# Optimization experiments

Measured on AMD Instinct MI355X. Metric: run time of the kernel, lower is better.

The kernel has to match this reference:

```python
import jax, jax.numpy as jnp
import numpy as np

B, S, T = 32, 2048, 768
NH, DH, DHID = 8, 96, 384  # num_heads, head_dim, hidden_dim=4*head_dim


def setup_inputs() -> dict:
    key = jax.random.key(0)
    k = jax.random.split(key, 7)
    token_embeddings = jax.random.normal(k[0], (B, S, T), dtype=jnp.float32)
    attention_mask = jnp.ones((B, S), dtype=jnp.float32)
    # per-head Linear params, stacked on a leading head axis (PyTorch default-ish init scale)
    P_w = jax.random.normal(k[1], (NH, T, DH), dtype=jnp.float32) * (1.0 / np.sqrt(T))
    P_b = jax.random.normal(k[2], (NH, DH), dtype=jnp.float32) * 0.01
    W1_w = jax.random.normal(k[3], (NH, DH, DHID), dtype=jnp.float32) * (1.0 / np.sqrt(DH))
    W1_b = jax.random.normal(k[4], (NH, DHID), dtype=jnp.float32) * 0.01
    W2_w = jax.random.normal(k[5], (NH, DHID, DH), dtype=jnp.float32) * (1.0 / np.sqrt(DHID))
    W2_b = jax.random.normal(k[6], (NH, DH), dtype=jnp.float32) * 0.01
    return {
        'token_embeddings': token_embeddings,
        'attention_mask': attention_mask,
        'P_w': P_w, 'P_b': P_b,
        'W1_w': W1_w, 'W1_b': W1_b,
        'W2_w': W2_w, 'W2_b': W2_b,
    }


def reference(token_embeddings, attention_mask, P_w, P_b, W1_w, W1_b, W2_w, W2_b):
    # Batched over heads instead of the original Python loop; same math per head.
    # H_i = P_i(H): (B, NH, S, DH)
    Hi = jnp.einsum('bst,htd->bhsd', token_embeddings, P_w) + P_b[None, :, None, :]
    # A_i = W2_i(relu(W1_i(H_i))): (B, NH, S, DH)
    A = jax.nn.relu(jnp.einsum('bhsd,hde->bhse', Hi, W1_w) + W1_b[None, :, None, :])
    A = jnp.einsum('bhse,hed->bhsd', A, W2_w) + W2_b[None, :, None, :]
    # masked softmax over the sequence axis (log(mask) adds -inf at padded tokens)
    log_mask = jnp.log(attention_mask)[:, None, :, None]  # (B,1,S,1)
    A = jax.nn.softmax(A + log_mask, axis=2)
    # weighted sum over tokens: (B, NH, DH)
    v = jnp.sum(Hi * A, axis=2)
    # concat heads -> (B, NH*DH) == (B, sentence_dim)
    return v.reshape(v.shape[0], NH * DH)
```

## Files before the change

kernel.cpp:

```cpp
#include <hip/hip_runtime.h>
#include <cstdint>
#include <cstddef>

#define Bsz   32
#define Ssz   2048
#define Tsz   768
#define NH    8
#define DH    96
#define DHID  384
#define Ncols (NH*DH)

using u16 = unsigned short;
typedef __bf16 bf16x8 __attribute__((ext_vector_type(8)));
typedef __bf16 bf16x4 __attribute__((ext_vector_type(4)));
typedef float  f32x4  __attribute__((ext_vector_type(4)));

__device__ __forceinline__ u16 f2bn(float f) {
  __bf16 h = (__bf16)f;
  return __builtin_bit_cast(u16, h);
}
__device__ __forceinline__ float b2f(u16 u) {
  return __builtin_bit_cast(float, (uint32_t)u << 16);
}

typedef const __attribute__((address_space(1))) void* gas_t;
typedef __attribute__((address_space(3))) void* las_t;
__device__ __forceinline__ void gload16(const void* g, void* s) {
  __builtin_amdgcn_global_load_lds((gas_t)g, (las_t)s, 16, 0, 0);
}

__global__ __launch_bounds__(256) void k_pack(const float* __restrict__ Pw,
    const float* __restrict__ W1w, const float* __restrict__ W2w,
    u16* __restrict__ B1t, u16* __restrict__ W1t, u16* __restrict__ W2t)
{
  int i = blockIdx.x * 256 + threadIdx.x;
  if (i < 589824) {
    int n = i / 768, k = i % 768;
    int h = n / 96, d = n % 96;
    B1t[i] = f2bn(Pw[(size_t)h*73728 + (size_t)k*96 + d]);
  } else if (i < 589824 + 294912) {
    int j = i - 589824;
    int h = j / 36864, r = j % 36864;
    int n = r / 96, k = r % 96;
    W1t[j] = f2bn(W1w[(size_t)h*36864 + (size_t)k*384 + n]);
  } else if (i < 589824 + 2*294912) {
    int q = i - 589824 - 294912;
    int h = q / 36864, r = q % 36864;
    int n = r / 384, k = r % 384;
    W2t[q] = f2bn(W2w[(size_t)h*36864 + (size_t)k*96 + n]);
  }
}

__global__ __launch_bounds__(256, 2) void k_gemm1(const float* __restrict__ emb,
    const u16* __restrict__ B1t, const float* __restrict__ Pb, u16* __restrict__ Hi)
{
  __shared__ u16 As[256*64];
  __shared__ u16 Bs[128*64];
  const int tid  = threadIdx.x;
  const int lane = tid & 63;
  const int w    = tid >> 6;
  const int wr = w >> 1, wc = w & 1;
  const int L = blockIdx.x;
  const int widx = (L & 7) * 192 + (L >> 3);
  const int bm = widx / 6, bn = widx % 6;
  const int l15 = lane & 15, lg = lane >> 4;

  const int srow   = lane >> 3;
  const int schunk = lane & 7;
  const int brow_in = lane >> 3;
  const int bchunk  = lane & 7;

  f32x4 acc[8][4] = {};

  for (int kt = 0; kt < 12; ++kt) {
    const int k0 = kt * 64;
    #pragma unroll
    for (int i = 0; i < 4; ++i) {
      const int row = (w*4 + i)*8 + brow_in;
      const int lc  = bchunk ^ brow_in;
      gload16(B1t + (size_t)(bn*128 + row)*Tsz + k0 + lc*8,
              &Bs[(w*4 + i)*512]);
    }
    #pragma unroll
    for (int i = 0; i < 8; ++i) {
      const int row = w*64 + i*8 + srow;
      const float* src = emb + (size_t)(bm*256 + row)*Tsz + k0 + schunk*8;
      float4 v0 = *reinterpret_cast<const float4*>(src);
      float4 v1 = *reinterpret_cast<const float4*>(src + 4);
      bf16x8 af;
      af[0] = (__bf16)v0.x; af[1] = (__bf16)v0.y; af[2] = (__bf16)v0.z; af[3] = (__bf16)v0.w;
      af[4] = (__bf16)v1.x; af[5] = (__bf16)v1.y; af[6] = (__bf16)v1.z; af[7] = (__bf16)v1.w;
      const int phys = schunk ^ (row & 7);
      *reinterpret_cast<bf16x8*>(&As[row*64 + phys*8]) = af;
    }
    __syncthreads();

    #pragma unroll
    for (int kk = 0; kk < 2; ++kk) {
      const int clog = kk*4 + lg;
      bf16x8 b[4];
      #pragma unroll
      for (int c = 0; c < 4; ++c) {
        const int Rb = wc*64 + c*16 + l15;
        b[c] = *reinterpret_cast<const bf16x8*>(&Bs[Rb*64 + (clog ^ (Rb & 7))*8]);
      }
      bf16x8 a[8];
      #pragma unroll
      for (int m = 0; m < 8; ++m) {
        const int R = wr*128 + m*16 + l15;
        a[m] = *reinterpret_cast<const bf16x8*>(&As[R*64 + (clog ^ (R & 7))*8]);
      }
      #pragma unroll
      for (int m = 0; m < 8; ++m)
        #pragma unroll
        for (int c = 0; c < 4; ++c)
          acc[m][c] = __builtin_amdgcn_mfma_f32_16x16x32_bf16(a[m], b[c], acc[m][c], 0, 0, 0);
    }
    __syncthreads();
  }
  #pragma unroll
  for (int c = 0; c < 4; ++c) {
    int col = bn*128 + wc*64 + c*16 + l15;
    float bias = Pb[col];
    #pragma unroll
    for (int m = 0; m < 8; ++m) {
      int row0 = bm*256 + wr*128 + m*16 + lg*4;
      #pragma unroll
      for (int j = 0; j < 4; ++j)
        Hi[(size_t)(row0 + j)*Ncols + col] = f2bn(acc[m][c][j] + bias);
    }
  }
}

__global__ __launch_bounds__(256, 1) void k_ffn_pool(
    const u16* __restrict__ Hi, const u16* __restrict__ W1t, const u16* __restrict__ W2t,
    const float* __restrict__ b1, const float* __restrict__ b2v, const float* __restrict__ mask,
    float* __restrict__ out)
{
  __shared__ u16 W2s[96][392];
  __shared__ u16 Zb[4][2][16][40];
  __shared__ float mb[4][96], lb[4][96], ab[4][96];

  const int tid = threadIdx.x, lane = tid & 63, w = tid >> 6;
  const int l15 = lane & 15, lg = lane >> 4;
  const int h = blockIdx.x, b = blockIdx.y;

  const u16* W1h = W1t + (size_t)h * DHID * DH;
  const u16* W2h = W2t + (size_t)h * DH * DHID;
  const float* b1h = b1 + h * DHID;

  for (int i = tid; i < 96*48; i += 256) {
    int r = i / 48, g = i % 48;
    uint4 v = *reinterpret_cast<const uint4*>(W2h + (size_t)r*DHID + g*8);
    *reinterpret_cast<uint4*>(&W2s[r][g*8]) = v;
  }
  __syncthreads();

  float b2s[6];
  #pragma unroll
  for (int ct = 0; ct < 6; ++ct) b2s[ct] = b2v[h*DH + ct*16 + l15];

  float Mr[6], Lr[6], Ar[6];
  #pragma unroll
  for (int ct = 0; ct < 6; ++ct) { Mr[ct] = -3.4e38f; Lr[ct] = 0.f; Ar[ct] = 0.f; }

  #pragma unroll 1
  for (int pass = 0; pass < 8; ++pass) {
    const size_t prow = (size_t)b*Ssz + (size_t)w*512 + (size_t)pass*64;

    bf16x8 hifr[4][3];
    #pragma unroll
    for (int s = 0; s < 4; ++s)
      #pragma unroll
      for (int ks = 0; ks < 3; ++ks)
        hifr[s][ks] = *reinterpret_cast<const bf16x8*>(
            Hi + (prow + s*16 + l15)*Ncols + h*DH + ks*32 + lg*8);

    f32x4 lgt[4][6] = {};

    #pragma unroll 2
    for (int c = 0; c < 12; ++c) {
      bf16x8 a1c[2][3];
      #pragma unroll
      for (int t = 0; t < 2; ++t)
        #pragma unroll
        for (int ks = 0; ks < 3; ++ks)
          a1c[t][ks] = *reinterpret_cast<const bf16x8*>(
              W1h + (size_t)(c*32 + t*16 + l15)*DH + ks*32 + lg*8);
      float4 bc0 = *reinterpret_cast<const float4*>(b1h + c*32 + lg*4);
      float4 bc1 = *reinterpret_cast<const float4*>(b1h + c*32 + 16 + lg*4);
      bf16x8 b2fr[6];
      #pragma unroll
      for (int ct = 0; ct < 6; ++ct)
        b2fr[ct] = *reinterpret_cast<const bf16x8*>(&W2s[ct*16 + l15][c*32 + lg*8]);

      #pragma unroll
      for (int bi = 0; bi < 2; ++bi) {
        f32x4 z[2][2];
        #pragma unroll
        for (int sl = 0; sl < 2; ++sl) {
          z[sl][0] = f32x4{}; z[sl][1] = f32x4{};
          #pragma unroll
          for (int ks = 0; ks < 3; ++ks) {
            z[sl][0] = __builtin_amdgcn_mfma_f32_16x16x32_bf16(a1c[0][ks], hifr[bi*2+sl][ks], z[sl][0], 0, 0, 0);
            z[sl][1] = __builtin_amdgcn_mfma_f32_16x16x32_bf16(a1c[1][ks], hifr[bi*2+sl][ks], z[sl][1], 0, 0, 0);
          }
        }
        #pragma unroll
        for (int sl = 0; sl < 2; ++sl) {
          bf16x4 p0, p1;
          p0[0] = (__bf16)fmaxf(z[sl][0][0] + bc0.x, 0.f);
          p0[1] = (__bf16)fmaxf(z[sl][0][1] + bc0.y, 0.f);
          p0[2] = (__bf16)fmaxf(z[sl][0][2] + bc0.z, 0.f);
          p0[3] = (__bf16)fmaxf(z[sl][0][3] + bc0.w, 0.f);
          p1[0] = (__bf16)fmaxf(z[sl][1][0] + bc1.x, 0.f);
          p1[1] = (__bf16)fmaxf(z[sl][1][1] + bc1.y, 0.f);
          p1[2] = (__bf16)fmaxf(z[sl][1][2] + bc1.z, 0.f);
          p1[3] = (__bf16)fmaxf(z[sl][1][3] + bc1.w, 0.f);
          *reinterpret_cast<uint2*>(&Zb[w][sl][l15][lg*4])      = __builtin_bit_cast(uint2, p0);
          *reinterpret_cast<uint2*>(&Zb[w][sl][l15][16 + lg*4]) = __builtin_bit_cast(uint2, p1);
        }
        #pragma unroll
        for (int sl = 0; sl < 2; ++sl) {
          bf16x8 zf = *reinterpret_cast<const bf16x8*>(&Zb[w][sl][l15][lg*8]);
          #pragma unroll
          for (int ct = 0; ct < 6; ++ct)
            lgt[bi*2+sl][ct] = __builtin_amdgcn_mfma_f32_16x16x32_bf16(zf, b2fr[ct], lgt[bi*2+sl][ct], 0, 0, 0);
        }
      }
    }

    float lmv[4][4];
    #pragma unroll
    for (int s = 0; s < 4; ++s) {
      float4 mk = *reinterpret_cast<const float4*>(&mask[prow + s*16 + lg*4]);
      lmv[s][0] = __logf(mk.x); lmv[s][1] = __logf(mk.y);
      lmv[s][2] = __logf(mk.z); lmv[s][3] = __logf(mk.w);
    }
    float G[4][6][4];
    #pragma unroll
    for (int s = 0; s < 4; ++s)
      #pragma unroll
      for (int ct = 0; ct < 6; ++ct)
        #pragma unroll
        for (int j = 0; j < 4; ++j)
          G[s][ct][j] = b2f(Hi[(prow + s*16 + lg*4 + j)*Ncols + h*DH + ct*16 + l15]);

    #pragma unroll
    for (int ct = 0; ct < 6; ++ct) {
      float av[4][4];
      float m16 = -3.4e38f;
      #pragma unroll
      for (int s = 0; s < 4; ++s)
        #pragma unroll
        for (int j = 0; j < 4; ++j) {
          av[s][j] = lgt[s][ct][j] + b2s[ct] + lmv[s][j];
          m16 = fmaxf(m16, av[s][j]);
        }
      m16 = fmaxf(m16, __shfl_xor(m16, 16));
      m16 = fmaxf(m16, __shfl_xor(m16, 32));
      float l16 = 0.f, a16 = 0.f;
      #pragma unroll
      for (int s = 0; s < 4; ++s)
        #pragma unroll
        for (int j = 0; j < 4; ++j) {
          float p = __expf(av[s][j] - m16);
          l16 += p;
          a16 += p * G[s][ct][j];
        }
      l16 += __shfl_xor(l16, 16); l16 += __shfl_xor(l16, 32);
      a16 += __shfl_xor(a16, 16); a16 += __shfl_xor(a16, 32);
      float M2 = fmaxf(Mr[ct], m16);
      float eo = __expf(Mr[ct] - M2), en = __expf(m16 - M2);
      Lr[ct] = Lr[ct]*eo + l16*en;
      Ar[ct] = Ar[ct]*eo + a16*en;
      Mr[ct] = M2;
    }
  }

  if (lane < 16) {
    #pragma unroll
    for (int ct = 0; ct < 6; ++ct) {
      mb[w][ct*16 + l15] = Mr[ct];
      lb[w][ct*16 + l15] = Lr[ct];
      ab[w][ct*16 + l15] = Ar[ct];
    }
  }
  __syncthreads();
  if (tid < 96) {
    float m = fmaxf(fmaxf(mb[0][tid], mb[1][tid]), fmaxf(mb[2][tid], mb[3][tid]));
    float l = 0.f, a = 0.f;
    #pragma unroll
    for (int q = 0; q < 4; ++q) {
      float sc = __expf(mb[q][tid] - m);
      l += lb[q][tid] * sc;
      a += ab[q][tid] * sc;
    }
    out[(size_t)b * Ncols + h*DH + tid] = a / l;
  }
}

extern "C" void kernel_launch(void* const* d_in, const int* in_sizes, int n_in,
                              void* d_out, int out_size, void* d_ws, size_t ws_size,
                              hipStream_t stream)
{
  const float* emb  = (const float*)d_in[0];
  const float* mask = (const float*)d_in[1];
  const float* Pw   = (const float*)d_in[2];
  const float* Pb   = (const float*)d_in[3];
  const float* W1w  = (const float*)d_in[4];
  const float* W1b  = (const float*)d_in[5];
  const float* W2w  = (const float*)d_in[6];
  const float* W2b  = (const float*)d_in[7];
  float* out = (float*)d_out;

  char* ws = (char*)d_ws;
  u16*   Hi  = (u16*)(ws);
  u16*   B1t = (u16*)(ws + 100663296ull);
  u16*   W1t = (u16*)(ws + 101842944ull);
  u16*   W2t = (u16*)(ws + 102432768ull);

  k_pack<<<dim3(4608), dim3(256), 0, stream>>>(Pw, W1w, W2w, B1t, W1t, W2t);
  k_gemm1<<<dim3(1536), dim3(256), 0, stream>>>(emb, B1t, Pb, Hi);
  k_ffn_pool<<<dim3(8, 32), dim3(256), 0, stream>>>(Hi, W1t, W2t, W1b, W2b, mask, out);
}
```

Baseline: 284.0 us.

## Prefetch next K tile into registers during MFMA compute in projection GEMM

The projection GEMM now loads the next K-tile of embeddings (converted to bf16) and of the packed weight into registers while MFMAs run on the current LDS tile. It then writes them to LDS after a barrier. This replaces the direct global-to-LDS load for the weight tile and the load-then-sync-then-compute sequence, so global memory latency is meant to hide behind compute. It raises register pressure (12 extra bf16x8 vectors per thread alongside a 128-float accumulator) and adds a second barrier per iteration.

```diff
diff --git a/kernel.cpp b/kernel.cpp
--- a/kernel.cpp
+++ b/kernel.cpp
@@ -21,12 +21,6 @@
 }
 __device__ __forceinline__ float b2f(u16 u) {
   return __builtin_bit_cast(float, (uint32_t)u << 16);
-}
-
-typedef const __attribute__((address_space(1))) void* gas_t;
-typedef __attribute__((address_space(3))) void* las_t;
-__device__ __forceinline__ void gload16(const void* g, void* s) {
-  __builtin_amdgcn_global_load_lds((gas_t)g, (las_t)s, 16, 0, 0);
 }
 
 __global__ __launch_bounds__(256) void k_pack(const float* __restrict__ Pw,
@@ -67,20 +61,13 @@
 
   const int srow   = lane >> 3;
   const int schunk = lane & 7;
-  const int brow_in = lane >> 3;
-  const int bchunk  = lane & 7;
-
-  f32x4 acc[8][4] = {};
-
-  for (int kt = 0; kt < 12; ++kt) {
+  const int wchunk = schunk ^ srow;
+
+  bf16x8 pa[8];
+  bf16x8 pb[4];
+
+  auto load_tile = [&](int kt) {
     const int k0 = kt * 64;
-    #pragma unroll
-    for (int i = 0; i < 4; ++i) {
-      const int row = (w*4 + i)*8 + brow_in;
-      const int lc  = bchunk ^ brow_in;
-      gload16(B1t + (size_t)(bn*128 + row)*Tsz + k0 + lc*8,
-              &Bs[(w*4 + i)*512]);
-    }
     #pragma unroll
     for (int i = 0; i < 8; ++i) {
       const int row = w*64 + i*8 + srow;
@@ -90,11 +77,37 @@
       bf16x8 af;
       af[0] = (__bf16)v0.x; af[1] = (__bf16)v0.y; af[2] = (__bf16)v0.z; af[3] = (__bf16)v0.w;
       af[4] = (__bf16)v1.x; af[5] = (__bf16)v1.y; af[6] = (__bf16)v1.z; af[7] = (__bf16)v1.w;
-      const int phys = schunk ^ (row & 7);
-      *reinterpret_cast<bf16x8*>(&As[row*64 + phys*8]) = af;
-    }
-    __syncthreads();
-
+      pa[i] = af;
+    }
+    #pragma unroll
+    for (int i = 0; i < 4; ++i) {
+      const int row = w*32 + i*8 + srow;
+      pb[i] = *reinterpret_cast<const bf16x8*>(
+          B1t + (size_t)(bn*128 + row)*Tsz + k0 + schunk*8);
+    }
+  };
+  auto write_tile = [&]() {
+    #pragma unroll
+    for (int i = 0; i < 8; ++i) {
+      const int row = w*64 + i*8 + srow;
+      *reinterpret_cast<bf16x8*>(&As[row*64 + wchunk*8]) = pa[i];
+    }
+    #pragma unroll
+    for (int i = 0; i < 4; ++i) {
+      const int row = w*32 + i*8 + srow;
+      *reinterpret_cast<bf16x8*>(&Bs[row*64 + wchunk*8]) = pb[i];
+    }
+  };
+
+  f32x4 acc[8][4] = {};
+
+  load_tile(0);
+  write_tile();
+  __syncthreads();
+
+  #pragma unroll 1
+  for (int kt = 0; kt < 12; ++kt) {
+    if (kt < 11) load_tile(kt + 1);
     #pragma unroll
     for (int kk = 0; kk < 2; ++kk) {
       const int clog = kk*4 + lg;
@@ -117,7 +130,12 @@
           acc[m][c] = __builtin_amdgcn_mfma_f32_16x16x32_bf16(a[m], b[c], acc[m][c], 0, 0, 0);
     }
     __syncthreads();
-  }
+    if (kt < 11) {
+      write_tile();
+      __syncthreads();
+    }
+  }
+
   #pragma unroll
   for (int c = 0; c < 4; ++c) {
     int col = bn*128 + wc*64 + c*16 + l15;
```

Result: faster. 274.5 us (-3.4%).
